# Kernel optimization log

Hardware: AMD Instinct MI355X
Metric: run time of the kernel (lower is better)

Reference implementation:

```python
import jax, jax.numpy as jnp
import numpy as np

B, K, D = 8192, 50, 64
NU, NV = 100000, 100000


def setup_inputs() -> dict:
    key = jax.random.key(0)
    ks = jax.random.split(key, 9)
    nodes = jax.random.randint(ks[0], (B,), 0, NU)
    history = jax.random.randint(ks[1], (B, K), 0, NV)
    degrees = jax.random.randint(ks[2], (B,), 1, K + 1)  # 1..K actual neighbors per node
    u_to_e = jax.random.normal(ks[3], (NU, D), dtype=jnp.float32)
    v_to_e = jax.random.normal(ks[4], (NV, D), dtype=jnp.float32)
    s1 = 1.0 / np.sqrt(2 * D)
    s2 = 1.0 / np.sqrt(D)
    att1_w = jax.random.normal(ks[5], (D, 2 * D), dtype=jnp.float32) * s1
    att2_w = jax.random.normal(ks[6], (D, D), dtype=jnp.float32) * s2
    att3_w = jax.random.normal(ks[7], (1, D), dtype=jnp.float32) * s2
    return {
        "nodes": nodes, "history": history, "degrees": degrees,
        "u_to_e": u_to_e, "v_to_e": v_to_e,
        "att1_w": att1_w, "att1_b": jnp.zeros((D,), jnp.float32),
        "att2_w": att2_w, "att2_b": jnp.zeros((D,), jnp.float32),
        "att3_w": att3_w, "att3_b": jnp.zeros((1,), jnp.float32),
    }


def reference(nodes, history, degrees, u_to_e, v_to_e,
              att1_w, att1_b, att2_w, att2_b, att3_w, att3_b):
    # uv=True: neighbors are items (v_to_e), self representation from u_to_e.
    neigh = v_to_e[history]                      # [B, K, D] gathered neighbor embeddings
    self_e = u_to_e[nodes]                       # [B, D]
    self_rep = jnp.broadcast_to(self_e[:, None, :], neigh.shape)
    x = jnp.concatenate([neigh, self_rep], axis=-1)        # [B, K, 2D]
    h = jax.nn.relu(jnp.einsum('bkf,df->bkd', x, att1_w) + att1_b)
    h = jax.nn.relu(jnp.einsum('bkd,ed->bke', h, att2_w) + att2_b)
    logits = (jnp.einsum('bkd,od->bko', h, att3_w) + att3_b)[..., 0]  # [B, K]
    # Softmax over the true (ragged) neighbor set only.
    mask = jnp.arange(K)[None, :] < degrees[:, None]       # [B, K] bool
    logits = jnp.where(mask, logits, -1e9)
    att = jax.nn.softmax(logits, axis=1) * mask            # [B, K]
    return jnp.einsum('bkd,bk->bd', neigh, att)            # [B, D]
```

## Files before the change

### kernel.cpp

```cpp
#include <hip/hip_runtime.h>
#include <cstdint>
#include <cstddef>

constexpr int D = 64;
constexpr int TWO_D = 128;

typedef __attribute__((ext_vector_type(8))) short bf16x8;
typedef __attribute__((ext_vector_type(4))) float f32x4;
typedef __attribute__((ext_vector_type(4))) unsigned short u16x4;

static __device__ __forceinline__ short f2bf(float x) {
    unsigned u = __builtin_bit_cast(unsigned, x);
    u += 0x7fffu + ((u >> 16) & 1u);
    return (short)(u >> 16);
}
static __device__ __forceinline__ float bf2f(unsigned short h) {
    return __builtin_bit_cast(float, ((unsigned)h) << 16);
}
static __device__ __forceinline__ float readlane_f(float v, int lane) {
    return __builtin_bit_cast(float,
        __builtin_amdgcn_readlane(__builtin_bit_cast(int, v), lane));
}

__global__ __launch_bounds__(256) void proj_gemm(
    const float* __restrict__ v_to_e, const float* __restrict__ u_to_e,
    const int* __restrict__ nodes,
    const float* __restrict__ att1_w, const float* __restrict__ att1_b,
    const float* __restrict__ att2_w,
    unsigned short* __restrict__ P16, float* __restrict__ S,
    unsigned short* __restrict__ W2F, unsigned short* __restrict__ V16,
    int NV, int Bn, int nPB)
{
    const int tid = threadIdx.x;

    if ((int)blockIdx.x == nPB + (Bn + 63) / 64) {
        if (tid < 64) {
            const int plg = tid >> 4, plc = tid & 15;
#pragma unroll
            for (int tc = 0; tc < 4; ++tc)
#pragma unroll
                for (int ks = 0; ks < 2; ++ks) {
                    const float* src =
                        att2_w + (tc * 16 + plc) * D + ks * 32 + plg * 8;
                    const float4 a = *(const float4*)src;
                    const float4 c = *(const float4*)(src + 4);
                    bf16x8 f;
                    f[0] = f2bf(a.x); f[1] = f2bf(a.y);
                    f[2] = f2bf(a.z); f[3] = f2bf(a.w);
                    f[4] = f2bf(c.x); f[5] = f2bf(c.y);
                    f[6] = f2bf(c.z); f[7] = f2bf(c.w);
                    *(bf16x8*)(W2F + ((size_t)(tc * 2 + ks) * 64 + tid) * 8) = f;
                }
        }
        return;
    }

    constexpr int ST = 68;
    __shared__ float xs[64 * ST];
    __shared__ float ws[64 * ST];

    const bool isS = ((int)blockIdx.x >= nPB);
    const int base = (isS ? ((int)blockIdx.x - nPB) : (int)blockIdx.x) * 64;
    const int nRows = isS ? Bn : NV;
    const int woff  = isS ? D : 0;
    const float* X  = isS ? u_to_e : v_to_e;

#pragma unroll
    for (int it = 0; it < 4; ++it) {
        const int flat = it * 256 + tid;
        const int dd = flat >> 4, f4 = flat & 15;
        const float4 w = *(const float4*)(att1_w + dd * TWO_D + woff + f4 * 4);
        ws[(f4 * 4 + 0) * ST + dd] = w.x;
        ws[(f4 * 4 + 1) * ST + dd] = w.y;
        ws[(f4 * 4 + 2) * ST + dd] = w.z;
        ws[(f4 * 4 + 3) * ST + dd] = w.w;
    }
#pragma unroll
    for (int it = 0; it < 4; ++it) {
        const int flat = it * 256 + tid;
        const int r = flat >> 4, f4 = flat & 15;
        int gr = base + r;
        if (gr >= nRows) gr = nRows - 1;
        const int row = isS ? nodes[gr] : gr;
        const float4 x = *(const float4*)(X + (size_t)row * D + f4 * 4);
        xs[(f4 * 4 + 0) * ST + r] = x.x;
        xs[(f4 * 4 + 1) * ST + r] = x.y;
        xs[(f4 * 4 + 2) * ST + r] = x.z;
        xs[(f4 * 4 + 3) * ST + r] = x.w;
        if (!isS) {
            u16x4 o;
            o[0] = (unsigned short)f2bf(x.x);
            o[1] = (unsigned short)f2bf(x.y);
            o[2] = (unsigned short)f2bf(x.z);
            o[3] = (unsigned short)f2bf(x.w);
            *(u16x4*)(V16 + (size_t)gr * D + f4 * 4) = o;
        }
    }
    __syncthreads();

    const int d0 = (tid & 15) * 4;
    const int r0 = (tid >> 4) * 4;
    float acc[4][4];
#pragma unroll
    for (int i = 0; i < 4; ++i)
#pragma unroll
        for (int j = 0; j < 4; ++j) acc[i][j] = 0.f;

#pragma unroll 8
    for (int f = 0; f < D; ++f) {
        const float4 w = *(const float4*)&ws[f * ST + d0];
        const float4 x = *(const float4*)&xs[f * ST + r0];
        const float wv[4] = {w.x, w.y, w.z, w.w};
        const float xv[4] = {x.x, x.y, x.z, x.w};
#pragma unroll
        for (int ri = 0; ri < 4; ++ri)
#pragma unroll
            for (int di = 0; di < 4; ++di)
                acc[ri][di] += xv[ri] * wv[di];
    }

    if (isS) {
        float bv[4];
#pragma unroll
        for (int di = 0; di < 4; ++di) bv[di] = att1_b[d0 + di];
#pragma unroll
        for (int ri = 0; ri < 4; ++ri) {
            const int gr = base + r0 + ri;
            if (gr < nRows) {
                float4 o = {acc[ri][0] + bv[0], acc[ri][1] + bv[1],
                            acc[ri][2] + bv[2], acc[ri][3] + bv[3]};
                *(float4*)(S + (size_t)gr * D + d0) = o;
            }
        }
    } else {
#pragma unroll
        for (int ri = 0; ri < 4; ++ri) {
            const int gr = base + r0 + ri;
            if (gr < nRows) {
                u16x4 o;
                o[0] = (unsigned short)f2bf(acc[ri][0]);
                o[1] = (unsigned short)f2bf(acc[ri][1]);
                o[2] = (unsigned short)f2bf(acc[ri][2]);
                o[3] = (unsigned short)f2bf(acc[ri][3]);
                *(u16x4*)(P16 + (size_t)gr * D + d0) = o;
            }
        }
    }
}

__global__ __launch_bounds__(256) void agg_mfma(
    const int* __restrict__ history, const int* __restrict__ degrees,
    const float* __restrict__ att2_b, const float* __restrict__ att3_w,
    const unsigned short* __restrict__ P16, const float* __restrict__ S,
    const unsigned short* __restrict__ W2F,
    const unsigned short* __restrict__ V16,
    float* __restrict__ out, int Bn, int K)
{
    __shared__ float red[4][64];
    __shared__ float mxs[4];
    __shared__ float sms[4];

    const int b     = (int)blockIdx.x;
    const int wslot = threadIdx.x >> 6;
    const int l     = threadIdx.x & 63;
    const int lg    = l >> 4;
    const int lc    = l & 15;
    const int deg   = degrees[b];
    const bool live = (wslot * 16 < deg);
    const bool act  = (wslot * 16 + lc < deg);

    int kk = wslot * 16 + lc;
    if (kk > K - 1) kk = K - 1;
    const int vrow = history[(size_t)b * K + kk];

    float vreg[16];
    if (live) {
#pragma unroll
        for (int j = 0; j < 16; ++j) {
            const int vk = __builtin_amdgcn_readlane(vrow, j);
            vreg[j] = bf2f(V16[(size_t)vk * D + l]);
        }
    }

    float m_w = -1e30f, ex = 0.f, od = 0.f;
    if (live) {
        const bf16x8 praw0 = *(const bf16x8*)(P16 + (size_t)vrow * D + lg * 8);
        const bf16x8 praw1 = *(const bf16x8*)(P16 + (size_t)vrow * D + 32 + lg * 8);
        const float* sp = S + (size_t)b * D;
        const float4 s00 = *(const float4*)(sp + lg * 8);
        const float4 s01 = *(const float4*)(sp + lg * 8 + 4);
        const float4 s10 = *(const float4*)(sp + 32 + lg * 8);
        const float4 s11 = *(const float4*)(sp + 32 + lg * 8 + 4);

        bf16x8 af0, af1;
        af0[0] = f2bf(fmaxf(bf2f((unsigned short)praw0[0]) + s00.x, 0.f));
        af0[1] = f2bf(fmaxf(bf2f((unsigned short)praw0[1]) + s00.y, 0.f));
        af0[2] = f2bf(fmaxf(bf2f((unsigned short)praw0[2]) + s00.z, 0.f));
        af0[3] = f2bf(fmaxf(bf2f((unsigned short)praw0[3]) + s00.w, 0.f));
        af0[4] = f2bf(fmaxf(bf2f((unsigned short)praw0[4]) + s01.x, 0.f));
        af0[5] = f2bf(fmaxf(bf2f((unsigned short)praw0[5]) + s01.y, 0.f));
        af0[6] = f2bf(fmaxf(bf2f((unsigned short)praw0[6]) + s01.z, 0.f));
        af0[7] = f2bf(fmaxf(bf2f((unsigned short)praw0[7]) + s01.w, 0.f));
        af1[0] = f2bf(fmaxf(bf2f((unsigned short)praw1[0]) + s10.x, 0.f));
        af1[1] = f2bf(fmaxf(bf2f((unsigned short)praw1[1]) + s10.y, 0.f));
        af1[2] = f2bf(fmaxf(bf2f((unsigned short)praw1[2]) + s10.z, 0.f));
        af1[3] = f2bf(fmaxf(bf2f((unsigned short)praw1[3]) + s10.w, 0.f));
        af1[4] = f2bf(fmaxf(bf2f((unsigned short)praw1[4]) + s11.x, 0.f));
        af1[5] = f2bf(fmaxf(bf2f((unsigned short)praw1[5]) + s11.y, 0.f));
        af1[6] = f2bf(fmaxf(bf2f((unsigned short)praw1[6]) + s11.z, 0.f));
        af1[7] = f2bf(fmaxf(bf2f((unsigned short)praw1[7]) + s11.w, 0.f));

        f32x4 acc[4];
#pragma unroll
        for (int tc = 0; tc < 4; ++tc) acc[tc] = (f32x4)0.f;
#pragma unroll
        for (int tc = 0; tc < 4; ++tc) {
            const bf16x8 w0 = *(const bf16x8*)(
                W2F + ((size_t)(tc * 2 + 0) * 64 + l) * 8);
            acc[tc] = __builtin_amdgcn_mfma_f32_16x16x32_bf16(
                w0, af0, acc[tc], 0, 0, 0);
            const bf16x8 w1 = *(const bf16x8*)(
                W2F + ((size_t)(tc * 2 + 1) * 64 + l) * 8);
            acc[tc] = __builtin_amdgcn_mfma_f32_16x16x32_bf16(
                w1, af1, acc[tc], 0, 0, 0);
        }

        float part = 0.f;
#pragma unroll
        for (int tc = 0; tc < 4; ++tc) {
            const float4 b2v = *(const float4*)(att2_b + tc * 16 + lg * 4);
            const float4 w3v = *(const float4*)(att3_w + tc * 16 + lg * 4);
            part += fmaxf(acc[tc][0] + b2v.x, 0.f) * w3v.x;
            part += fmaxf(acc[tc][1] + b2v.y, 0.f) * w3v.y;
            part += fmaxf(acc[tc][2] + b2v.z, 0.f) * w3v.z;
            part += fmaxf(acc[tc][3] + b2v.w, 0.f) * w3v.w;
        }
        part += __shfl_xor(part, 16);
        part += __shfl_xor(part, 32);
        const float logit = act ? part : -1e30f;

        m_w = logit;
#pragma unroll
        for (int off = 1; off < 16; off <<= 1)
            m_w = fmaxf(m_w, __shfl_xor(m_w, off));
        ex = act ? __expf(logit - m_w) : 0.f;
        float s_w = ex;
#pragma unroll
        for (int off = 1; off < 16; off <<= 1)
            s_w += __shfl_xor(s_w, off);
        if (l == 0) { mxs[wslot] = m_w; sms[wslot] = s_w; }

        float od0 = 0.f, od1 = 0.f;
#pragma unroll
        for (int j = 0; j < 16; j += 2) {
            od0 += readlane_f(ex, j)     * vreg[j];
            od1 += readlane_f(ex, j + 1) * vreg[j + 1];
        }
        od = od0 + od1;
    } else {
        if (l == 0) { mxs[wslot] = -1e30f; sms[wslot] = 0.f; }
    }

    __syncthreads();
    const float m = fmaxf(fmaxf(mxs[0], mxs[1]), fmaxf(mxs[2], mxs[3]));
    const float tot = sms[0] * __expf(mxs[0] - m) + sms[1] * __expf(mxs[1] - m)
                    + sms[2] * __expf(mxs[2] - m) + sms[3] * __expf(mxs[3] - m);
    const float scale = live ? __expf(m_w - m) / tot : 0.f;
    red[wslot][l] = od * scale;
    __syncthreads();
    if (wslot == 0)
        out[(size_t)b * D + l] =
            (red[0][l] + red[1][l]) + (red[2][l] + red[3][l]);
}

__global__ __launch_bounds__(256) void agg_fallback(
    const int* __restrict__ nodes, const int* __restrict__ history,
    const int* __restrict__ degrees,
    const float* __restrict__ u_to_e, const float* __restrict__ v_to_e,
    const float* __restrict__ att1_w, const float* __restrict__ att1_b,
    const float* __restrict__ att2_w, const float* __restrict__ att2_b,
    const float* __restrict__ att3_w, const float* __restrict__ att3_b,
    float* __restrict__ out, int Bn, int K)
{
    const int b    = (int)((blockIdx.x * blockDim.x + threadIdx.x) >> 6);
    const int lane = threadIdx.x & 63;
    if (b >= Bn) return;

    const int  deg    = degrees[b];
    const bool active = (lane < deg);
    const int  v      = history[(size_t)b * K + ((lane < K) ? lane : 0)];

    float h1[D];
    float vr[D];
    const float4* v4 = (const float4*)(v_to_e + (size_t)v * D);
#pragma unroll
    for (int i = 0; i < D / 4; ++i) {
        float4 t = v4[i];
        vr[4 * i + 0] = t.x; vr[4 * i + 1] = t.y;
        vr[4 * i + 2] = t.z; vr[4 * i + 3] = t.w;
    }
    const float* urow = u_to_e + (size_t)nodes[b] * D;
#pragma unroll
    for (int d = 0; d < D; ++d) {
        const float* w1 = att1_w + d * TWO_D;
        float a0 = att1_b[d], a1 = 0.f, a2 = 0.f, a3 = 0.f;
#pragma unroll
        for (int f = 0; f < D; f += 4) {
            a0 += vr[f + 0] * w1[f + 0];
            a1 += vr[f + 1] * w1[f + 1];
            a2 += vr[f + 2] * w1[f + 2];
            a3 += vr[f + 3] * w1[f + 3];
            a0 += urow[f + 0] * w1[D + f + 0];
            a1 += urow[f + 1] * w1[D + f + 1];
            a2 += urow[f + 2] * w1[D + f + 2];
            a3 += urow[f + 3] * w1[D + f + 3];
        }
        h1[d] = fmaxf((a0 + a1) + (a2 + a3), 0.f);
    }

    float logit = att3_b[0];
#pragma unroll 4
    for (int e = 0; e < D; ++e) {
        const float* w2r = att2_w + e * D;
        float a0 = 0.f, a1 = 0.f, a2 = 0.f, a3 = 0.f;
#pragma unroll
        for (int dd = 0; dd < D; dd += 4) {
            a0 += h1[dd + 0] * w2r[dd + 0];
            a1 += h1[dd + 1] * w2r[dd + 1];
            a2 += h1[dd + 2] * w2r[dd + 2];
            a3 += h1[dd + 3] * w2r[dd + 3];
        }
        float h2 = (a0 + a1) + (a2 + a3) + att2_b[e];
        logit += fmaxf(h2, 0.f) * att3_w[e];
    }

    float ml = active ? logit : -1e30f;
#pragma unroll
    for (int off = 32; off > 0; off >>= 1) ml = fmaxf(ml, __shfl_xor(ml, off));
    const float ex = active ? __expf(logit - ml) : 0.f;
    float smv = ex;
#pragma unroll
    for (int off = 32; off > 0; off >>= 1) smv += __shfl_xor(smv, off);
    const float att = ex / smv;

    float acc = 0.f;
    for (int kk = 0; kk < deg; ++kk) {
        const float a  = __shfl(att, kk);
        const int   vk = __shfl(v, kk);
        acc += a * v_to_e[(size_t)vk * D + lane];
    }
    out[(size_t)b * D + lane] = acc;
}

extern "C" void kernel_launch(void* const* d_in, const int* in_sizes, int n_in,
                              void* d_out, int out_size, void* d_ws, size_t ws_size,
                              hipStream_t stream)
{
    const int*   nodes   = (const int*)d_in[0];
    const int*   history = (const int*)d_in[1];
    const int*   degrees = (const int*)d_in[2];
    const float* u_to_e  = (const float*)d_in[3];
    const float* v_to_e  = (const float*)d_in[4];
    const float* att1_w  = (const float*)d_in[5];
    const float* att1_b  = (const float*)d_in[6];
    const float* att2_w  = (const float*)d_in[7];
    const float* att2_b  = (const float*)d_in[8];
    const float* att3_w  = (const float*)d_in[9];
    const float* att3_b  = (const float*)d_in[10];
    float*       out     = (float*)d_out;

    const int Bn = in_sizes[0];
    const int K  = in_sizes[1] / Bn;
    const int NV = in_sizes[4] / D;

    const size_t p16_bytes = (size_t)NV * D * sizeof(unsigned short);
    const size_t s_bytes   = (size_t)Bn * D * sizeof(float);
    const size_t w2f_bytes = (size_t)8 * 64 * 8 * sizeof(unsigned short);
    const size_t v16_bytes = (size_t)NV * D * sizeof(unsigned short);
    const size_t need = p16_bytes + s_bytes + w2f_bytes + v16_bytes;

    if (ws_size >= need) {
        unsigned short* P16 = (unsigned short*)d_ws;
        float* S = (float*)((char*)d_ws + p16_bytes);
        unsigned short* W2F = (unsigned short*)((char*)d_ws + p16_bytes + s_bytes);
        unsigned short* V16 = (unsigned short*)((char*)d_ws + p16_bytes + s_bytes + w2f_bytes);
        const int nPB = (NV + 63) / 64;
        const int nSB = (Bn + 63) / 64;
        proj_gemm<<<nPB + nSB + 1, 256, 0, stream>>>(
            v_to_e, u_to_e, nodes, att1_w, att1_b, att2_w,
            P16, S, W2F, V16, NV, Bn, nPB);
        agg_mfma<<<Bn, 256, 0, stream>>>(
            history, degrees, att2_b, att3_w,
            P16, S, W2F, V16, out, Bn, K);
    } else {
        const int agg_blocks = (Bn * 64 + 255) / 256;
        agg_fallback<<<agg_blocks, 256, 0, stream>>>(
            nodes, history, degrees, u_to_e, v_to_e,
            att1_w, att1_b, att2_w, att2_b, att3_w, att3_b,
            out, Bn, K);
    }
}
```

Before: 52.32 us.

## Vectorize neighbor row gather and fuse MFMA epilogue to cut registers

```diff
diff --git a/kernel.cpp b/kernel.cpp
--- a/kernel.cpp
+++ b/kernel.cpp
@@ -16,10 +16,6 @@
 }
 static __device__ __forceinline__ float bf2f(unsigned short h) {
     return __builtin_bit_cast(float, ((unsigned)h) << 16);
-}
-static __device__ __forceinline__ float readlane_f(float v, int lane) {
-    return __builtin_bit_cast(float,
-        __builtin_amdgcn_readlane(__builtin_bit_cast(int, v), lane));
 }
 
 __global__ __launch_bounds__(256) void proj_gemm(
@@ -148,7 +144,7 @@
     }
 }
 
-__global__ __launch_bounds__(256) void agg_mfma(
+__global__ __launch_bounds__(256, 8) void agg_mfma(
     const int* __restrict__ history, const int* __restrict__ degrees,
     const float* __restrict__ att2_b, const float* __restrict__ att3_w,
     const unsigned short* __restrict__ P16, const float* __restrict__ S,
@@ -173,16 +169,17 @@
     if (kk > K - 1) kk = K - 1;
     const int vrow = history[(size_t)b * K + kk];
 
-    float vreg[16];
+    u16x4 vr4[4];
     if (live) {
 #pragma unroll
-        for (int j = 0; j < 16; ++j) {
-            const int vk = __builtin_amdgcn_readlane(vrow, j);
-            vreg[j] = bf2f(V16[(size_t)vk * D + l]);
-        }
-    }
-
-    float m_w = -1e30f, ex = 0.f, od = 0.f;
+        for (int jj = 0; jj < 4; ++jj) {
+            const int row = __shfl(vrow, jj * 4 + lg);
+            vr4[jj] = *(const u16x4*)(V16 + (size_t)row * D + lc * 4);
+        }
+    }
+
+    float m_w = -1e30f, ex = 0.f;
+    float4 acc4 = {0.f, 0.f, 0.f, 0.f};
     if (live) {
         const bf16x8 praw0 = *(const bf16x8*)(P16 + (size_t)vrow * D + lg * 8);
         const bf16x8 praw1 = *(const bf16x8*)(P16 + (size_t)vrow * D + 32 + lg * 8);
@@ -210,30 +207,22 @@
         af1[6] = f2bf(fmaxf(bf2f((unsigned short)praw1[6]) + s11.z, 0.f));
         af1[7] = f2bf(fmaxf(bf2f((unsigned short)praw1[7]) + s11.w, 0.f));
 
-        f32x4 acc[4];
-#pragma unroll
-        for (int tc = 0; tc < 4; ++tc) acc[tc] = (f32x4)0.f;
+        float part = 0.f;
 #pragma unroll
         for (int tc = 0; tc < 4; ++tc) {
+            f32x4 acc = (f32x4)0.f;
             const bf16x8 w0 = *(const bf16x8*)(
                 W2F + ((size_t)(tc * 2 + 0) * 64 + l) * 8);
-            acc[tc] = __builtin_amdgcn_mfma_f32_16x16x32_bf16(
-                w0, af0, acc[tc], 0, 0, 0);
+            acc = __builtin_amdgcn_mfma_f32_16x16x32_bf16(w0, af0, acc, 0, 0, 0);
             const bf16x8 w1 = *(const bf16x8*)(
                 W2F + ((size_t)(tc * 2 + 1) * 64 + l) * 8);
-            acc[tc] = __builtin_amdgcn_mfma_f32_16x16x32_bf16(
-                w1, af1, acc[tc], 0, 0, 0);
-        }
-
-        float part = 0.f;
-#pragma unroll
-        for (int tc = 0; tc < 4; ++tc) {
+            acc = __builtin_amdgcn_mfma_f32_16x16x32_bf16(w1, af1, acc, 0, 0, 0);
             const float4 b2v = *(const float4*)(att2_b + tc * 16 + lg * 4);
             const float4 w3v = *(const float4*)(att3_w + tc * 16 + lg * 4);
-            part += fmaxf(acc[tc][0] + b2v.x, 0.f) * w3v.x;
-            part += fmaxf(acc[tc][1] + b2v.y, 0.f) * w3v.y;
-            part += fmaxf(acc[tc][2] + b2v.z, 0.f) * w3v.z;
-            part += fmaxf(acc[tc][3] + b2v.w, 0.f) * w3v.w;
+            part += fmaxf(acc[0] + b2v.x, 0.f) * w3v.x;
+            part += fmaxf(acc[1] + b2v.y, 0.f) * w3v.y;
+            part += fmaxf(acc[2] + b2v.z, 0.f) * w3v.z;
+            part += fmaxf(acc[3] + b2v.w, 0.f) * w3v.w;
         }
         part += __shfl_xor(part, 16);
         part += __shfl_xor(part, 32);
@@ -250,13 +239,18 @@
             s_w += __shfl_xor(s_w, off);
         if (l == 0) { mxs[wslot] = m_w; sms[wslot] = s_w; }
 
-        float od0 = 0.f, od1 = 0.f;
-#pragma unroll
-        for (int j = 0; j < 16; j += 2) {
-            od0 += readlane_f(ex, j)     * vreg[j];
-            od1 += readlane_f(ex, j + 1) * vreg[j + 1];
-        }
-        od = od0 + od1;
+#pragma unroll
+        for (int jj = 0; jj < 4; ++jj) {
+            const float a = __shfl(ex, jj * 4 + lg);
+            acc4.x += a * bf2f(vr4[jj][0]);
+            acc4.y += a * bf2f(vr4[jj][1]);
+            acc4.z += a * bf2f(vr4[jj][2]);
+            acc4.w += a * bf2f(vr4[jj][3]);
+        }
+        acc4.x += __shfl_xor(acc4.x, 16); acc4.x += __shfl_xor(acc4.x, 32);
+        acc4.y += __shfl_xor(acc4.y, 16); acc4.y += __shfl_xor(acc4.y, 32);
+        acc4.z += __shfl_xor(acc4.z, 16); acc4.z += __shfl_xor(acc4.z, 32);
+        acc4.w += __shfl_xor(acc4.w, 16); acc4.w += __shfl_xor(acc4.w, 32);
     } else {
         if (l == 0) { mxs[wslot] = -1e30f; sms[wslot] = 0.f; }
     }
@@ -266,7 +260,10 @@
     const float tot = sms[0] * __expf(mxs[0] - m) + sms[1] * __expf(mxs[1] - m)
                     + sms[2] * __expf(mxs[2] - m) + sms[3] * __expf(mxs[3] - m);
     const float scale = live ? __expf(m_w - m) / tot : 0.f;
-    red[wslot][l] = od * scale;
+
+    const float comp = (lg == 0) ? acc4.x : (lg == 1) ? acc4.y
+                     : (lg == 2) ? acc4.z : acc4.w;
+    red[wslot][lc * 4 + lg] = comp * scale;
     __syncthreads();
     if (wslot == 0)
         out[(size_t)b * D + l] =
@@ -380,10 +377,11 @@
     const size_t need = p16_bytes + s_bytes + w2f_bytes + v16_bytes;
 
     if (ws_size >= need) {
-        unsigned short* P16 = (unsigned short*)d_ws;
-        float* S = (float*)((char*)d_ws + p16_bytes);
-        unsigned short* W2F = (unsigned short*)((char*)d_ws + p16_bytes + s_bytes);
-        unsigned short* V16 = (unsigned short*)((char*)d_ws + p16_bytes + s_bytes + w2f_bytes);
+        char* p = (char*)d_ws;
+        unsigned short* P16 = (unsigned short*)p;   p += p16_bytes;
+        float*          S   = (float*)p;            p += s_bytes;
+        unsigned short* W2F = (unsigned short*)p;   p += w2f_bytes;
+        unsigned short* V16 = (unsigned short*)p;
         const int nPB = (NV + 63) / 64;
         const int nSB = (Bn + 63) / 64;
         proj_gemm<<<nPB + nSB + 1, 256, 0, stream>>>(
```

Result: no change. 51.77 us (-1.1%).
